# Optimization experiments

Measured on AMD Instinct MI355X. Metric: run time of the kernel, lower is better.

Reference implementation:

```python
import jax, jax.numpy as jnp
import numpy as np

EMBED = 1024
HEADS = 16
HEAD_DIM = EMBED // HEADS


def setup_inputs() -> dict:
    key = jax.random.key(0)
    ks = jax.random.split(key, 8)
    N, S = 4, 2048
    inp = {
        "values": jax.random.normal(ks[0], (N, S, EMBED), jnp.float32),
        "keys": jax.random.normal(ks[1], (N, S, EMBED), jnp.float32),
        "queries": jax.random.normal(ks[2], (N, S, EMBED), jnp.float32),
        "mask": jnp.ones((N, S), jnp.int32),  # unused by the original forward
        # learned params (torch Linear: y = x @ W.T + b)
        "Wv": jax.random.normal(ks[3], (HEAD_DIM, HEAD_DIM), jnp.float32) / np.sqrt(HEAD_DIM),
        "Wk": jax.random.normal(ks[4], (HEAD_DIM, HEAD_DIM), jnp.float32) / np.sqrt(HEAD_DIM),
        "Wq": jax.random.normal(ks[5], (HEAD_DIM, HEAD_DIM), jnp.float32) / np.sqrt(HEAD_DIM),
        "Wo": jax.random.normal(ks[6], (EMBED, EMBED), jnp.float32) / np.sqrt(EMBED),
        "bo": jax.random.normal(ks[7], (EMBED,), jnp.float32) * 0.01,
    }
    return inp


def reference(values, keys, queries, mask, Wv, Wk, Wq, Wo, bo):
    N, S, _ = queries.shape
    # reshape to (N, len, heads, head_dim)
    v = values.reshape(N, S, HEADS, HEAD_DIM)
    k = keys.reshape(N, S, HEADS, HEAD_DIM)
    q = queries.reshape(N, S, HEADS, HEAD_DIM)
    # per-head linear projections (weights shared across heads), y = x @ W.T
    v = jnp.einsum('nlhd,ed->nlhe', v, Wv)
    k = jnp.einsum('nlhd,ed->nlhe', k, Wk)
    q = jnp.einsum('nlhd,ed->nlhe', q, Wq)
    # attention scores scaled by sqrt(embed_size), faithful to original
    scores = jnp.einsum('nqhd,nkhd->nhqk', q, k) / jnp.sqrt(jnp.float32(EMBED))
    attn = jax.nn.softmax(scores, axis=3)
    out = jnp.einsum('nhql,nlhd->nqhd', attn, v).reshape(N, S, EMBED)
    return out @ Wo.T + bo
```

## Files before the change

### kernel.cpp

```cpp
#include <hip/hip_runtime.h>


using f32x4  = __attribute__((ext_vector_type(4))) float;
using f32x16 = __attribute__((ext_vector_type(16))) float;
using bf16x8 = __attribute__((ext_vector_type(8))) __bf16;
using u32x4  = __attribute__((ext_vector_type(4))) unsigned int;
using u16x8  = __attribute__((ext_vector_type(8))) unsigned short;
typedef unsigned short u16;
typedef unsigned int   u32;
typedef unsigned long long u64;

#define SEQ 2048
#define EMB 1024
#define NHEADS 16
#define HDIM 64
#define NBATCH 4
#define NH 64

__device__ __forceinline__ u16 f2bf(float f) {
  u32 u = __builtin_bit_cast(u32, f);
  return (u16)((u + 0x7fffu + ((u >> 16) & 1u)) >> 16);
}

__device__ __forceinline__ f32x4 mfma16(bf16x8 a, bf16x8 b, f32x4 c) {
  return __builtin_amdgcn_mfma_f32_16x16x32_bf16(a, b, c, 0, 0, 0);
}

__device__ __forceinline__ f32x16 mfma32(bf16x8 a, bf16x8 b, f32x16 c) {
  return __builtin_amdgcn_mfma_f32_32x32x16_bf16(a, b, c, 0, 0, 0);
}

__device__ __forceinline__ bf16x8 cvt8(f32x4 a, f32x4 b) {
  u16x8 r;
  r[0] = f2bf(a[0]); r[1] = f2bf(a[1]); r[2] = f2bf(a[2]); r[3] = f2bf(a[3]);
  r[4] = f2bf(b[0]); r[5] = f2bf(b[1]); r[6] = f2bf(b[2]); r[7] = f2bf(b[3]);
  return __builtin_bit_cast(bf16x8, r);
}

__device__ __forceinline__ u32 cvtpk_bf16(float a, float b) {
  u32 d;
  asm("v_cvt_pk_bf16_f32 %0, %1, %2" : "=v"(d) : "v"(a), "v"(b));
  return d;
}

__device__ __forceinline__ float fexp2(float x) {
#if __has_builtin(__builtin_amdgcn_exp2f)
  return __builtin_amdgcn_exp2f(x);
#else
  return __expf(x * 0.6931471805599453f);
#endif
}

__device__ __forceinline__ void swap_words(u32 a, u32 b, int hi, u32& wlo, u32& whi) {
#if __has_builtin(__builtin_amdgcn_permlane32_swap)
  (void)hi;
  auto rr = __builtin_amdgcn_permlane32_swap((int)a, (int)b, false, false);
  wlo = (u32)rr[0];
  whi = (u32)rr[1];
#else
  u32 pa = (u32)__shfl_xor((int)a, 32);
  u32 pb = (u32)__shfl_xor((int)b, 32);
  wlo = hi ? pb : a;
  whi = hi ? b : pa;
#endif
}

__global__ __launch_bounds__(256) void proj_kernel(
    const float* __restrict__ Xq, const float* __restrict__ Xk, const float* __restrict__ Xv,
    const float* __restrict__ Wq, const float* __restrict__ Wk, const float* __restrict__ Wv,
    u16* __restrict__ Qp, u16* __restrict__ Kp, u16* __restrict__ Vp)
{
  int which = blockIdx.y;
  const float* X = which == 0 ? Xq : (which == 1 ? Xk : Xv);
  const float* W = which == 0 ? Wq : (which == 1 ? Wk : Wv);
  u16* Out = which == 0 ? Qp : (which == 1 ? Kp : Vp);
  float wscale = which == 0 ? 0.045084220027780106f : 1.0f;

  int t = threadIdx.x;
  int w = t >> 6, l = t & 63, l15 = l & 15, grp = l >> 4;
  int g0 = blockIdx.x * 64;

  bf16x8 wf[4][2];
#pragma unroll
  for (int nt = 0; nt < 4; nt++) {
    int c = nt * 16 + l15;
#pragma unroll
    for (int dc = 0; dc < 2; dc++) {
      const float* p = W + c * 64 + dc * 32 + grp * 8;
      f32x4 a = *(const f32x4*)p;
      f32x4 b = *(const f32x4*)(p + 4);
      a *= wscale; b *= wscale;
      wf[nt][dc] = cvt8(a, b);
    }
  }
  int grow = g0 + w * 16 + l15;
  const float* xr = X + (long)grow * 64;
  bf16x8 af[2];
#pragma unroll
  for (int dc = 0; dc < 2; dc++) {
    f32x4 a = *(const f32x4*)(xr + dc * 32 + grp * 8);
    f32x4 b = *(const f32x4*)(xr + dc * 32 + grp * 8 + 4);
    af[dc] = cvt8(a, b);
  }
  f32x4 acc[4] = {};
#pragma unroll
  for (int dc = 0; dc < 2; dc++)
#pragma unroll
    for (int nt = 0; nt < 4; nt++)
      acc[nt] = mfma16(af[dc], wf[nt][dc], acc[nt]);

#pragma unroll
  for (int r = 0; r < 4; r++) {
    int g = g0 + w * 16 + grp * 4 + r;
    int n = g >> 15;
    int s = (g >> 4) & 2047;
    int h = g & 15;
    u16* orow = Out + (((long)(n * NHEADS + h) * SEQ + s) << 6);
#pragma unroll
    for (int nt = 0; nt < 4; nt++)
      orow[nt * 16 + l15] = f2bf(acc[nt][r]);
  }
}

__global__ __launch_bounds__(256) void transpose_v(
    const u16* __restrict__ Vp, u16* __restrict__ Vt)
{
  int st = blockIdx.x;
  int nh = blockIdx.y;
  __shared__ u16 Vs[64 * 65];
  int t = threadIdx.x;
  const u16* src = Vp + ((long)nh * SEQ + st * 64) * 64;
#pragma unroll
  for (int p = 0; p < 2; p++) {
    int row = p * 32 + (t >> 3);
    int c0 = (t & 7) * 8;
    u32x4 u = *(const u32x4*)(src + row * 64 + c0);
    u16x8 v = __builtin_bit_cast(u16x8, u);
#pragma unroll
    for (int j = 0; j < 8; j++) Vs[(c0 + j) * 65 + row] = v[j];
  }
  __syncthreads();
  int e = t >> 2, k0 = (t & 3) * 16;
  u16x8 lo, hi;
#pragma unroll
  for (int j = 0; j < 8; j++) { lo[j] = Vs[e * 65 + k0 + j]; hi[j] = Vs[e * 65 + k0 + 8 + j]; }
  u16* dst = Vt + ((long)nh * 64 + e) * SEQ + st * 64 + k0;
  *(u32x4*)dst = __builtin_bit_cast(u32x4, lo);
  *(u32x4*)(dst + 8) = __builtin_bit_cast(u32x4, hi);
}

__global__ __launch_bounds__(256) void conv_wo(
    const float* __restrict__ Wo, u16* __restrict__ Wob)
{
  int i = (blockIdx.x * 256 + threadIdx.x) * 4;
  f32x4 v = *(const f32x4*)(Wo + i);
  u64 pk = (u64)f2bf(v[0]) | ((u64)f2bf(v[1]) << 16) |
           ((u64)f2bf(v[2]) << 32) | ((u64)f2bf(v[3]) << 48);
  *(u64*)(Wob + i) = pk;
}

__global__ __launch_bounds__(256, 3) void attn_kernel(
    const u16* __restrict__ Qp, const u16* __restrict__ Kp, const u16* __restrict__ Vt,
    u16* __restrict__ AO)
{
  int nh = blockIdx.x;
  int qb = blockIdx.y;
  int n = nh >> 4, h = nh & 15;

  __shared__ __align__(16) char smem[128 * 144];
  char* KsB = smem;
  char* VsB = smem + 8192;

  int t = threadIdx.x, w = t >> 6, l = t & 63;
  int l31 = l & 31, hi = l >> 5;

  long qrow = (long)nh * SEQ + qb * 128 + w * 32 + l31;
  const char* qbase = (const char*)Qp + qrow * 128;
  bf16x8 qf[4];
#pragma unroll
  for (int dc = 0; dc < 4; dc++)
    qf[dc] = __builtin_bit_cast(bf16x8, *(const u32x4*)(qbase + dc * 32 + hi * 16));

  f32x16 o0 = {}, o1 = {};
  float mrun = -1e30f, lrun = 0.f;

  const char* Kg = (const char*)(Kp + (long)nh * SEQ * 64);
  const char* Vg = (const char*)(Vt + (long)nh * 64 * SEQ);

  u32x4 kreg[2], vreg[2];
#pragma unroll
  for (int p = 0; p < 2; p++) {
    int chunk = p * 256 + t;
    int row = chunk >> 3, c = chunk & 7;
    kreg[p] = *(const u32x4*)(Kg + row * 128 + c * 16);
    vreg[p] = *(const u32x4*)(Vg + (long)row * 4096 + c * 16);
  }

  for (int kt = 0; kt < 32; kt++) {
    __syncthreads();
#pragma unroll
    for (int p = 0; p < 2; p++) {
      int chunk = p * 256 + t;
      int row = chunk >> 3, c = chunk & 7;
      int phys = row * 128 + ((c ^ (row & 7)) << 4);
      *(u32x4*)(KsB + phys) = kreg[p];
      *(u32x4*)(VsB + phys) = vreg[p];
    }
    __syncthreads();
    if (kt + 1 < 32) {
#pragma unroll
      for (int p = 0; p < 2; p++) {
        int chunk = p * 256 + t;
        int row = chunk >> 3, c = chunk & 7;
        kreg[p] = *(const u32x4*)(Kg + (long)(kt + 1) * 8192 + row * 128 + c * 16);
        vreg[p] = *(const u32x4*)(Vg + (long)row * 4096 + (kt + 1) * 128 + c * 16);
      }
    }

    f32x16 s0 = {}, s1 = {};
    __builtin_amdgcn_s_setprio(1);
#pragma unroll
    for (int dc = 0; dc < 4; dc++) {
      int cc = dc * 2 + hi;
      int r0 = l31;
      bf16x8 kf0 = __builtin_bit_cast(bf16x8,
          *(const u32x4*)(KsB + r0 * 128 + ((cc ^ (r0 & 7)) << 4)));
      s0 = mfma32(kf0, qf[dc], s0);
      int r1 = 32 + l31;
      bf16x8 kf1 = __builtin_bit_cast(bf16x8,
          *(const u32x4*)(KsB + r1 * 128 + ((cc ^ (r1 & 7)) << 4)));
      s1 = mfma32(kf1, qf[dc], s1);
    }
    __builtin_amdgcn_s_setprio(0);

    float mx = -1e30f;
#pragma unroll
    for (int r = 0; r < 8; r++)
      mx = fmaxf(mx, fmaxf(fmaxf(s0[2*r], s0[2*r+1]), fmaxf(s1[2*r], s1[2*r+1])));
    mx = fmaxf(mx, __shfl_xor(mx, 32));
    float mnew = fmaxf(mrun, mx);
    float scl = fexp2(mrun - mnew);
    mrun = mnew;
    lrun *= scl;
#pragma unroll
    for (int r = 0; r < 16; r++) { s0[r] = fexp2(s0[r] - mnew); lrun += s0[r]; }
#pragma unroll
    for (int r = 0; r < 16; r++) { s1[r] = fexp2(s1[r] - mnew); lrun += s1[r]; }
#pragma unroll
    for (int r = 0; r < 16; r++) { o0[r] *= scl; o1[r] *= scl; }

    bf16x8 pB[4];
    {
      u32 xw[8], wq[16];
#pragma unroll
      for (int i = 0; i < 8; i++) xw[i] = cvtpk_bf16(s0[2*i], s0[2*i+1]);
      swap_words(xw[0], xw[2], hi, wq[0],  wq[2]);
      swap_words(xw[1], xw[3], hi, wq[1],  wq[3]);
      swap_words(xw[4], xw[6], hi, wq[4],  wq[6]);
      swap_words(xw[5], xw[7], hi, wq[5],  wq[7]);
#pragma unroll
      for (int i = 0; i < 8; i++) xw[i] = cvtpk_bf16(s1[2*i], s1[2*i+1]);
      swap_words(xw[0], xw[2], hi, wq[8],  wq[10]);
      swap_words(xw[1], xw[3], hi, wq[9],  wq[11]);
      swap_words(xw[4], xw[6], hi, wq[12], wq[14]);
      swap_words(xw[5], xw[7], hi, wq[13], wq[15]);
#pragma unroll
      for (int kb = 0; kb < 4; kb++) {
        u32x4 v4 = { wq[kb*4+0], wq[kb*4+1], wq[kb*4+2], wq[kb*4+3] };
        pB[kb] = __builtin_bit_cast(bf16x8, v4);
      }
    }

    __builtin_amdgcn_s_setprio(1);
#pragma unroll
    for (int kb = 0; kb < 4; kb++) {
      int cc = kb * 2 + hi;
      int r0 = l31;
      bf16x8 vf0 = __builtin_bit_cast(bf16x8,
          *(const u32x4*)(VsB + r0 * 128 + ((cc ^ (r0 & 7)) << 4)));
      o0 = mfma32(vf0, pB[kb], o0);
      int r1 = 32 + l31;
      bf16x8 vf1 = __builtin_bit_cast(bf16x8,
          *(const u32x4*)(VsB + r1 * 128 + ((cc ^ (r1 & 7)) << 4)));
      o1 = mfma32(vf1, pB[kb], o1);
    }
    __builtin_amdgcn_s_setprio(0);
  }

  __syncthreads();
  lrun += __shfl_xor(lrun, 32);
  float inv = 1.0f / lrun;
  int qlocal = w * 32 + l31;
  char* OsmB = smem;
#pragma unroll
  for (int i = 0; i < 8; i++) {
    int e0 = ((2*i) & 3) + 8 * ((2*i) >> 2) + 4 * hi;
    u32 pk0 = cvtpk_bf16(o0[2*i] * inv, o0[2*i+1] * inv);
    *(u32*)(OsmB + qlocal * 144 + 2 * e0) = pk0;
    u32 pk1 = cvtpk_bf16(o1[2*i] * inv, o1[2*i+1] * inv);
    *(u32*)(OsmB + qlocal * 144 + 2 * (e0 + 32)) = pk1;
  }
  __syncthreads();
  int qr = t >> 1, half = t & 1;
  const char* src = OsmB + qr * 144 + half * 64;
  long qg = (long)qb * 128 + qr;
  char* dst = (char*)(AO + ((long)n * SEQ + qg) * EMB + h * 64 + half * 32);
#pragma unroll
  for (int j = 0; j < 4; j++)
    *(u32x4*)(dst + j * 16) = *(const u32x4*)(src + j * 16);
}

__global__ __launch_bounds__(256) void gemm_out(
    const u16* __restrict__ A, const u16* __restrict__ B,
    const float* __restrict__ bias, float* __restrict__ C)
{
  int bm = blockIdx.x, bn = blockIdx.y;
  __shared__ __align__(16) u16 As[4096];
  __shared__ __align__(16) u16 Bs[4096];
  int t = threadIdx.x, w = t >> 6, l = t & 63, l15 = l & 15, grp = l >> 4;
  int wm = w >> 1, wn = w & 1;
  f32x4 acc[4][4] = {};
  const char* Ab = (const char*)(A + (long)bm * 128 * 1024);
  const char* Bb = (const char*)(B + (long)bn * 128 * 1024);
  char* AsB = (char*)As;
  char* BsB = (char*)Bs;

  u32x4 areg[2], breg[2];
#pragma unroll
  for (int p = 0; p < 2; p++) {
    int chunk = p * 256 + t;
    int row = chunk >> 2, c = chunk & 3;
    areg[p] = *(const u32x4*)(Ab + (long)row * 2048 + c * 16);
    breg[p] = *(const u32x4*)(Bb + (long)row * 2048 + c * 16);
  }

  for (int kt = 0; kt < 32; kt++) {
    __syncthreads();
#pragma unroll
    for (int p = 0; p < 2; p++) {
      int chunk = p * 256 + t;
      int row = chunk >> 2, c = chunk & 3;
      int phys = row * 64 + ((c ^ ((row >> 1) & 3)) << 4);
      *(u32x4*)(AsB + phys) = areg[p];
      *(u32x4*)(BsB + phys) = breg[p];
    }
    __syncthreads();
    if (kt + 1 < 32) {
#pragma unroll
      for (int p = 0; p < 2; p++) {
        int chunk = p * 256 + t;
        int row = chunk >> 2, c = chunk & 3;
        areg[p] = *(const u32x4*)(Ab + (long)row * 2048 + (kt + 1) * 64 + c * 16);
        breg[p] = *(const u32x4*)(Bb + (long)row * 2048 + (kt + 1) * 64 + c * 16);
      }
    }
    bf16x8 af[4], bf_[4];
#pragma unroll
    for (int i = 0; i < 4; i++) {
      int row = wm * 64 + i * 16 + l15;
      af[i] = __builtin_bit_cast(bf16x8,
          *(const u32x4*)(AsB + row * 64 + ((grp ^ ((row >> 1) & 3)) << 4)));
      int rowb = wn * 64 + i * 16 + l15;
      bf_[i] = __builtin_bit_cast(bf16x8,
          *(const u32x4*)(BsB + rowb * 64 + ((grp ^ ((rowb >> 1) & 3)) << 4)));
    }
#pragma unroll
    for (int i = 0; i < 4; i++)
#pragma unroll
      for (int j = 0; j < 4; j++)
        acc[i][j] = mfma16(af[i], bf_[j], acc[i][j]);
  }

  float bv[4];
#pragma unroll
  for (int j = 0; j < 4; j++) bv[j] = bias[bn * 128 + wn * 64 + j * 16 + l15];
#pragma unroll
  for (int i = 0; i < 4; i++) {
#pragma unroll
    for (int r = 0; r < 4; r++) {
      long row = (long)bm * 128 + wm * 64 + i * 16 + grp * 4 + r;
      float* crow = C + row * 1024 + bn * 128 + wn * 64;
#pragma unroll
      for (int j = 0; j < 4; j++)
        crow[j * 16 + l15] = acc[i][j][r] + bv[j];
    }
  }
}

extern "C" void kernel_launch(void* const* d_in, const int* in_sizes, int n_in,
                              void* d_out, int out_size, void* d_ws, size_t ws_size,
                              hipStream_t stream)
{
  const float* Vx = (const float*)d_in[0];
  const float* Kx = (const float*)d_in[1];
  const float* Qx = (const float*)d_in[2];
  const float* Wv = (const float*)d_in[4];
  const float* Wk = (const float*)d_in[5];
  const float* Wq = (const float*)d_in[6];
  const float* Wo = (const float*)d_in[7];
  const float* bo = (const float*)d_in[8];
  float* out = (float*)d_out;
  char* ws = (char*)d_ws;

  u16* Qp  = (u16*)(ws);
  u16* Kp  = (u16*)(ws + (1L << 24));
  u16* Vt  = (u16*)(ws + (2L << 24));
  u16* Vp  = (u16*)(ws + (3L << 24));
  u16* AO  = Vp;
  u16* Wob = (u16*)(ws + (4L << 24));

  proj_kernel<<<dim3(2048, 3), 256, 0, stream>>>(Qx, Kx, Vx, Wq, Wk, Wv, Qp, Kp, Vp);
  transpose_v<<<dim3(32, 64), 256, 0, stream>>>(Vp, Vt);
  conv_wo<<<1024, 256, 0, stream>>>(Wo, Wob);
  attn_kernel<<<dim3(64, 16), 256, 0, stream>>>(Qp, Kp, Vt, AO);
  gemm_out<<<dim3(64, 8), 256, 0, stream>>>(AO, Wob, bo, out);
}
```

Before: 198.9 us.

## Double-buffer LDS tiles in attention and output GEMM, add lazy softmax rescale

Attention and the output GEMM now use two LDS buffers. The next tile is written to the spare buffer while the current one is consumed, which cuts each iteration's two barriers to one. Attention also skips rescaling the output accumulator unless the row max grows by more than a threshold, and uses tree reductions for the row max and row sum. The bf16 conversions switch to the packed convert instruction. The lazy rescale lets exponents run up to 2^8 before renormalising, which slightly changes numerics. The larger LDS footprint may lower occupancy.

```diff
diff --git a/kernel.cpp b/kernel.cpp
--- a/kernel.cpp
+++ b/kernel.cpp
@@ -22,25 +22,27 @@
   return (u16)((u + 0x7fffu + ((u >> 16) & 1u)) >> 16);
 }
 
-__device__ __forceinline__ f32x4 mfma16(bf16x8 a, bf16x8 b, f32x4 c) {
-  return __builtin_amdgcn_mfma_f32_16x16x32_bf16(a, b, c, 0, 0, 0);
-}
-
-__device__ __forceinline__ f32x16 mfma32(bf16x8 a, bf16x8 b, f32x16 c) {
-  return __builtin_amdgcn_mfma_f32_32x32x16_bf16(a, b, c, 0, 0, 0);
-}
-
-__device__ __forceinline__ bf16x8 cvt8(f32x4 a, f32x4 b) {
-  u16x8 r;
-  r[0] = f2bf(a[0]); r[1] = f2bf(a[1]); r[2] = f2bf(a[2]); r[3] = f2bf(a[3]);
-  r[4] = f2bf(b[0]); r[5] = f2bf(b[1]); r[6] = f2bf(b[2]); r[7] = f2bf(b[3]);
-  return __builtin_bit_cast(bf16x8, r);
-}
-
 __device__ __forceinline__ u32 cvtpk_bf16(float a, float b) {
   u32 d;
   asm("v_cvt_pk_bf16_f32 %0, %1, %2" : "=v"(d) : "v"(a), "v"(b));
   return d;
+}
+
+__device__ __forceinline__ f32x4 mfma16(bf16x8 a, bf16x8 b, f32x4 c) {
+  return __builtin_amdgcn_mfma_f32_16x16x32_bf16(a, b, c, 0, 0, 0);
+}
+
+__device__ __forceinline__ f32x16 mfma32(bf16x8 a, bf16x8 b, f32x16 c) {
+  return __builtin_amdgcn_mfma_f32_32x32x16_bf16(a, b, c, 0, 0, 0);
+}
+
+__device__ __forceinline__ bf16x8 cvt8(f32x4 a, f32x4 b) {
+  u32x4 r;
+  r[0] = cvtpk_bf16(a[0], a[1]);
+  r[1] = cvtpk_bf16(a[2], a[3]);
+  r[2] = cvtpk_bf16(b[0], b[1]);
+  r[3] = cvtpk_bf16(b[2], b[3]);
+  return __builtin_bit_cast(bf16x8, r);
 }
 
 __device__ __forceinline__ float fexp2(float x) {
@@ -154,8 +156,9 @@
 {
   int i = (blockIdx.x * 256 + threadIdx.x) * 4;
   f32x4 v = *(const f32x4*)(Wo + i);
-  u64 pk = (u64)f2bf(v[0]) | ((u64)f2bf(v[1]) << 16) |
-           ((u64)f2bf(v[2]) << 32) | ((u64)f2bf(v[3]) << 48);
+  u32 w0 = cvtpk_bf16(v[0], v[1]);
+  u32 w1 = cvtpk_bf16(v[2], v[3]);
+  u64 pk = (u64)w0 | ((u64)w1 << 32);
   *(u64*)(Wob + i) = pk;
 }
 
@@ -167,9 +170,7 @@
   int qb = blockIdx.y;
   int n = nh >> 4, h = nh & 15;
 
-  __shared__ __align__(16) char smem[128 * 144];
-  char* KsB = smem;
-  char* VsB = smem + 8192;
+  __shared__ __align__(16) char smem[32768];
 
   int t = threadIdx.x, w = t >> 6, l = t & 63;
   int l31 = l & 31, hi = l >> 5;
@@ -187,44 +188,39 @@
   const char* Kg = (const char*)(Kp + (long)nh * SEQ * 64);
   const char* Vg = (const char*)(Vt + (long)nh * 64 * SEQ);
 
+  int sr0 = t >> 3, sc = t & 7;
+  int sr1 = sr0 + 32;
+  int sphys0 = sr0 * 128 + ((sc ^ (sr0 & 7)) << 4);
+  int sphys1 = sr1 * 128 + ((sc ^ (sr1 & 7)) << 4);
+
   u32x4 kreg[2], vreg[2];
-#pragma unroll
-  for (int p = 0; p < 2; p++) {
-    int chunk = p * 256 + t;
-    int row = chunk >> 3, c = chunk & 7;
-    kreg[p] = *(const u32x4*)(Kg + row * 128 + c * 16);
-    vreg[p] = *(const u32x4*)(Vg + (long)row * 4096 + c * 16);
-  }
+  kreg[0] = *(const u32x4*)(Kg + sr0 * 128 + sc * 16);
+  kreg[1] = *(const u32x4*)(Kg + sr1 * 128 + sc * 16);
+  vreg[0] = *(const u32x4*)(Vg + (long)sr0 * 4096 + sc * 16);
+  vreg[1] = *(const u32x4*)(Vg + (long)sr1 * 4096 + sc * 16);
+  *(u32x4*)(smem + sphys0) = kreg[0];
+  *(u32x4*)(smem + sphys1) = kreg[1];
+  *(u32x4*)(smem + 8192 + sphys0) = vreg[0];
+  *(u32x4*)(smem + 8192 + sphys1) = vreg[1];
+  kreg[0] = *(const u32x4*)(Kg + 8192 + sr0 * 128 + sc * 16);
+  kreg[1] = *(const u32x4*)(Kg + 8192 + sr1 * 128 + sc * 16);
+  vreg[0] = *(const u32x4*)(Vg + (long)sr0 * 4096 + 128 + sc * 16);
+  vreg[1] = *(const u32x4*)(Vg + (long)sr1 * 4096 + 128 + sc * 16);
+  __syncthreads();
 
   for (int kt = 0; kt < 32; kt++) {
-    __syncthreads();
-#pragma unroll
-    for (int p = 0; p < 2; p++) {
-      int chunk = p * 256 + t;
-      int row = chunk >> 3, c = chunk & 7;
-      int phys = row * 128 + ((c ^ (row & 7)) << 4);
-      *(u32x4*)(KsB + phys) = kreg[p];
-      *(u32x4*)(VsB + phys) = vreg[p];
-    }
-    __syncthreads();
-    if (kt + 1 < 32) {
-#pragma unroll
-      for (int p = 0; p < 2; p++) {
-        int chunk = p * 256 + t;
-        int row = chunk >> 3, c = chunk & 7;
-        kreg[p] = *(const u32x4*)(Kg + (long)(kt + 1) * 8192 + row * 128 + c * 16);
-        vreg[p] = *(const u32x4*)(Vg + (long)row * 4096 + (kt + 1) * 128 + c * 16);
-      }
-    }
+    const char* cur = smem + ((kt & 1) << 14);
+    char* nxt = smem + (((kt + 1) & 1) << 14);
+    const char* KsB = cur;
+    const char* VsB = cur + 8192;
 
     f32x16 s0 = {}, s1 = {};
     __builtin_amdgcn_s_setprio(1);
 #pragma unroll
     for (int dc = 0; dc < 4; dc++) {
       int cc = dc * 2 + hi;
-      int r0 = l31;
       bf16x8 kf0 = __builtin_bit_cast(bf16x8,
-          *(const u32x4*)(KsB + r0 * 128 + ((cc ^ (r0 & 7)) << 4)));
+          *(const u32x4*)(KsB + l31 * 128 + ((cc ^ (l31 & 7)) << 4)));
       s0 = mfma32(kf0, qf[dc], s0);
       int r1 = 32 + l31;
       bf16x8 kf1 = __builtin_bit_cast(bf16x8,
@@ -233,40 +229,71 @@
     }
     __builtin_amdgcn_s_setprio(0);
 
-    float mx = -1e30f;
-#pragma unroll
-    for (int r = 0; r < 8; r++)
-      mx = fmaxf(mx, fmaxf(fmaxf(s0[2*r], s0[2*r+1]), fmaxf(s1[2*r], s1[2*r+1])));
+    if (kt + 1 < 32) {
+      *(u32x4*)(nxt + sphys0) = kreg[0];
+      *(u32x4*)(nxt + sphys1) = kreg[1];
+      *(u32x4*)(nxt + 8192 + sphys0) = vreg[0];
+      *(u32x4*)(nxt + 8192 + sphys1) = vreg[1];
+      if (kt + 2 < 32) {
+        const char* Kt = Kg + (long)(kt + 2) * 8192;
+        kreg[0] = *(const u32x4*)(Kt + sr0 * 128 + sc * 16);
+        kreg[1] = *(const u32x4*)(Kt + sr1 * 128 + sc * 16);
+        vreg[0] = *(const u32x4*)(Vg + (long)sr0 * 4096 + (kt + 2) * 128 + sc * 16);
+        vreg[1] = *(const u32x4*)(Vg + (long)sr1 * 4096 + (kt + 2) * 128 + sc * 16);
+      }
+    }
+
+    float m0 = fmaxf(s0[0], s1[0]), m1 = fmaxf(s0[1], s1[1]);
+    float m2 = fmaxf(s0[2], s1[2]), m3 = fmaxf(s0[3], s1[3]);
+#pragma unroll
+    for (int r = 4; r < 16; r += 4) {
+      m0 = fmaxf(m0, fmaxf(s0[r], s1[r]));
+      m1 = fmaxf(m1, fmaxf(s0[r + 1], s1[r + 1]));
+      m2 = fmaxf(m2, fmaxf(s0[r + 2], s1[r + 2]));
+      m3 = fmaxf(m3, fmaxf(s0[r + 3], s1[r + 3]));
+    }
+    float mx = fmaxf(fmaxf(m0, m1), fmaxf(m2, m3));
     mx = fmaxf(mx, __shfl_xor(mx, 32));
-    float mnew = fmaxf(mrun, mx);
-    float scl = fexp2(mrun - mnew);
-    mrun = mnew;
-    lrun *= scl;
-#pragma unroll
-    for (int r = 0; r < 16; r++) { s0[r] = fexp2(s0[r] - mnew); lrun += s0[r]; }
-#pragma unroll
-    for (int r = 0; r < 16; r++) { s1[r] = fexp2(s1[r] - mnew); lrun += s1[r]; }
-#pragma unroll
-    for (int r = 0; r < 16; r++) { o0[r] *= scl; o1[r] *= scl; }
+
+    if (__any(mx > mrun + 8.0f)) {
+      float mnew = fmaxf(mrun, mx);
+      float scl = fexp2(mrun - mnew);
+      mrun = mnew;
+      lrun *= scl;
+#pragma unroll
+      for (int r = 0; r < 16; r++) { o0[r] *= scl; o1[r] *= scl; }
+    }
+#pragma unroll
+    for (int r = 0; r < 16; r++) s0[r] = fexp2(s0[r] - mrun);
+#pragma unroll
+    for (int r = 0; r < 16; r++) s1[r] = fexp2(s1[r] - mrun);
+
+    {
+      f32x16 sv = s0 + s1;
+      f32x4 q4 = { sv[0] + sv[4], sv[1] + sv[5], sv[2] + sv[6], sv[3] + sv[7] };
+      f32x4 q5 = { sv[8] + sv[12], sv[9] + sv[13], sv[10] + sv[14], sv[11] + sv[15] };
+      f32x4 q6 = q4 + q5;
+      lrun += (q6[0] + q6[1]) + (q6[2] + q6[3]);
+    }
 
     bf16x8 pB[4];
     {
       u32 xw[8], wq[16];
 #pragma unroll
-      for (int i = 0; i < 8; i++) xw[i] = cvtpk_bf16(s0[2*i], s0[2*i+1]);
-      swap_words(xw[0], xw[2], hi, wq[0],  wq[2]);
-      swap_words(xw[1], xw[3], hi, wq[1],  wq[3]);
-      swap_words(xw[4], xw[6], hi, wq[4],  wq[6]);
-      swap_words(xw[5], xw[7], hi, wq[5],  wq[7]);
-#pragma unroll
-      for (int i = 0; i < 8; i++) xw[i] = cvtpk_bf16(s1[2*i], s1[2*i+1]);
-      swap_words(xw[0], xw[2], hi, wq[8],  wq[10]);
-      swap_words(xw[1], xw[3], hi, wq[9],  wq[11]);
+      for (int i = 0; i < 8; i++) xw[i] = cvtpk_bf16(s0[2 * i], s0[2 * i + 1]);
+      swap_words(xw[0], xw[2], hi, wq[0], wq[2]);
+      swap_words(xw[1], xw[3], hi, wq[1], wq[3]);
+      swap_words(xw[4], xw[6], hi, wq[4], wq[6]);
+      swap_words(xw[5], xw[7], hi, wq[5], wq[7]);
+#pragma unroll
+      for (int i = 0; i < 8; i++) xw[i] = cvtpk_bf16(s1[2 * i], s1[2 * i + 1]);
+      swap_words(xw[0], xw[2], hi, wq[8], wq[10]);
+      swap_words(xw[1], xw[3], hi, wq[9], wq[11]);
       swap_words(xw[4], xw[6], hi, wq[12], wq[14]);
       swap_words(xw[5], xw[7], hi, wq[13], wq[15]);
 #pragma unroll
       for (int kb = 0; kb < 4; kb++) {
-        u32x4 v4 = { wq[kb*4+0], wq[kb*4+1], wq[kb*4+2], wq[kb*4+3] };
+        u32x4 v4 = { wq[kb * 4 + 0], wq[kb * 4 + 1], wq[kb * 4 + 2], wq[kb * 4 + 3] };
         pB[kb] = __builtin_bit_cast(bf16x8, v4);
       }
     }
@@ -275,9 +302,8 @@
 #pragma unroll
     for (int kb = 0; kb < 4; kb++) {
       int cc = kb * 2 + hi;
-      int r0 = l31;
       bf16x8 vf0 = __builtin_bit_cast(bf16x8,
-          *(const u32x4*)(VsB + r0 * 128 + ((cc ^ (r0 & 7)) << 4)));
+          *(const u32x4*)(VsB + l31 * 128 + ((cc ^ (l31 & 7)) << 4)));
       o0 = mfma32(vf0, pB[kb], o0);
       int r1 = 32 + l31;
       bf16x8 vf1 = __builtin_bit_cast(bf16x8,
@@ -285,19 +311,20 @@
       o1 = mfma32(vf1, pB[kb], o1);
     }
     __builtin_amdgcn_s_setprio(0);
-  }
-
-  __syncthreads();
+
+    __syncthreads();
+  }
+
   lrun += __shfl_xor(lrun, 32);
   float inv = 1.0f / lrun;
   int qlocal = w * 32 + l31;
   char* OsmB = smem;
 #pragma unroll
   for (int i = 0; i < 8; i++) {
-    int e0 = ((2*i) & 3) + 8 * ((2*i) >> 2) + 4 * hi;
-    u32 pk0 = cvtpk_bf16(o0[2*i] * inv, o0[2*i+1] * inv);
+    int e0 = ((2 * i) & 3) + 8 * ((2 * i) >> 2) + 4 * hi;
+    u32 pk0 = cvtpk_bf16(o0[2 * i] * inv, o0[2 * i + 1] * inv);
     *(u32*)(OsmB + qlocal * 144 + 2 * e0) = pk0;
-    u32 pk1 = cvtpk_bf16(o1[2*i] * inv, o1[2*i+1] * inv);
+    u32 pk1 = cvtpk_bf16(o1[2 * i] * inv, o1[2 * i + 1] * inv);
     *(u32*)(OsmB + qlocal * 144 + 2 * (e0 + 32)) = pk1;
   }
   __syncthreads();
@@ -315,45 +342,38 @@
     const float* __restrict__ bias, float* __restrict__ C)
 {
   int bm = blockIdx.x, bn = blockIdx.y;
-  __shared__ __align__(16) u16 As[4096];
-  __shared__ __align__(16) u16 Bs[4096];
+  __shared__ __align__(16) char gsm[32768];
   int t = threadIdx.x, w = t >> 6, l = t & 63, l15 = l & 15, grp = l >> 4;
   int wm = w >> 1, wn = w & 1;
   f32x4 acc[4][4] = {};
   const char* Ab = (const char*)(A + (long)bm * 128 * 1024);
   const char* Bb = (const char*)(B + (long)bn * 128 * 1024);
-  char* AsB = (char*)As;
-  char* BsB = (char*)Bs;
+
+  int srow = t >> 2, sc2 = t & 3;
+  int srow1 = srow + 64;
+  int sp0 = srow * 64 + ((sc2 ^ ((srow >> 1) & 3)) << 4);
+  int sp1 = srow1 * 64 + ((sc2 ^ ((srow1 >> 1) & 3)) << 4);
 
   u32x4 areg[2], breg[2];
-#pragma unroll
-  for (int p = 0; p < 2; p++) {
-    int chunk = p * 256 + t;
-    int row = chunk >> 2, c = chunk & 3;
-    areg[p] = *(const u32x4*)(Ab + (long)row * 2048 + c * 16);
-    breg[p] = *(const u32x4*)(Bb + (long)row * 2048 + c * 16);
-  }
+  areg[0] = *(const u32x4*)(Ab + (long)srow * 2048 + sc2 * 16);
+  areg[1] = *(const u32x4*)(Ab + (long)srow1 * 2048 + sc2 * 16);
+  breg[0] = *(const u32x4*)(Bb + (long)srow * 2048 + sc2 * 16);
+  breg[1] = *(const u32x4*)(Bb + (long)srow1 * 2048 + sc2 * 16);
+  *(u32x4*)(gsm + sp0) = areg[0];
+  *(u32x4*)(gsm + sp1) = areg[1];
+  *(u32x4*)(gsm + 8192 + sp0) = breg[0];
+  *(u32x4*)(gsm + 8192 + sp1) = breg[1];
+  areg[0] = *(const u32x4*)(Ab + (long)srow * 2048 + 64 + sc2 * 16);
+  areg[1] = *(const u32x4*)(Ab + (long)srow1 * 2048 + 64 + sc2 * 16);
+  breg[0] = *(const u32x4*)(Bb + (long)srow * 2048 + 64 + sc2 * 16);
+  breg[1] = *(const u32x4*)(Bb + (long)srow1 * 2048 + 64 + sc2 * 16);
+  __syncthreads();
 
   for (int kt = 0; kt < 32; kt++) {
-    __syncthreads();
-#pragma unroll
-    for (int p = 0; p < 2; p++) {
-      int chunk = p * 256 + t;
-      int row = chunk >> 2, c = chunk & 3;
-      int phys = row * 64 + ((c ^ ((row >> 1) & 3)) << 4);
-      *(u32x4*)(AsB + phys) = areg[p];
-      *(u32x4*)(BsB + phys) = breg[p];
-    }
-    __syncthreads();
-    if (kt + 1 < 32) {
-#pragma unroll
-      for (int p = 0; p < 2; p++) {
-        int chunk = p * 256 + t;
-        int row = chunk >> 2, c = chunk & 3;
-        areg[p] = *(const u32x4*)(Ab + (long)row * 2048 + (kt + 1) * 64 + c * 16);
-        breg[p] = *(const u32x4*)(Bb + (long)row * 2048 + (kt + 1) * 64 + c * 16);
-      }
-    }
+    const char* AsB = gsm + ((kt & 1) << 14);
+    const char* BsB = AsB + 8192;
+    char* nxt = gsm + (((kt + 1) & 1) << 14);
+
     bf16x8 af[4], bf_[4];
 #pragma unroll
     for (int i = 0; i < 4; i++) {
@@ -364,11 +384,29 @@
       bf_[i] = __builtin_bit_cast(bf16x8,
           *(const u32x4*)(BsB + rowb * 64 + ((grp ^ ((rowb >> 1) & 3)) << 4)));
     }
+
+    if (kt + 1 < 32) {
+      *(u32x4*)(nxt + sp0) = areg[0];
+      *(u32x4*)(nxt + sp1) = areg[1];
+      *(u32x4*)(nxt + 8192 + sp0) = breg[0];
+      *(u32x4*)(nxt + 8192 + sp1) = breg[1];
+      if (kt + 2 < 32) {
+        areg[0] = *(const u32x4*)(Ab + (long)srow * 2048 + (kt + 2) * 64 + sc2 * 16);
+        areg[1] = *(const u32x4*)(Ab + (long)srow1 * 2048 + (kt + 2) * 64 + sc2 * 16);
+        breg[0] = *(const u32x4*)(Bb + (long)srow * 2048 + (kt + 2) * 64 + sc2 * 16);
+        breg[1] = *(const u32x4*)(Bb + (long)srow1 * 2048 + (kt + 2) * 64 + sc2 * 16);
+      }
+    }
+
+    __builtin_amdgcn_s_setprio(1);
 #pragma unroll
     for (int i = 0; i < 4; i++)
 #pragma unroll
       for (int j = 0; j < 4; j++)
         acc[i][j] = mfma16(af[i], bf_[j], acc[i][j]);
+    __builtin_amdgcn_s_setprio(0);
+
+    __syncthreads();
   }
 
   float bv[4];
```

New measurement: 190.0 us. 1.05x faster.
